# Optimization experiments

Hardware: AMD Instinct MI355X
Metric: run time of the kernel (lower is better)

## Reference

```python
import jax, jax.numpy as jnp
import numpy as np

B, S, D, H = 2, 2048, 2048, 16
HD = D // H


def setup_inputs() -> dict:
    key = jax.random.key(0)
    ks = jax.random.split(key, 9)
    s = 1.0 / np.sqrt(D)
    return {
        "hidden_states": jax.random.normal(ks[0], (B, S, D), dtype=jnp.float32),
        "attention_mask": jnp.ones((B, 1, 1, S), dtype=jnp.int32),
        "Wq": jax.random.normal(ks[1], (D, D), dtype=jnp.float32) * s,
        "bq": jnp.zeros((D,), dtype=jnp.float32),
        "Wk": jax.random.normal(ks[2], (D, D), dtype=jnp.float32) * s,
        "bk": jnp.zeros((D,), dtype=jnp.float32),
        "Wv": jax.random.normal(ks[3], (D, D), dtype=jnp.float32) * s,
        "bv": jnp.zeros((D,), dtype=jnp.float32),
        "Wo": jax.random.normal(ks[4], (D, D), dtype=jnp.float32) * s,
        "bo": jnp.zeros((D,), dtype=jnp.float32),
    }


def reference(hidden_states, attention_mask, Wq, bq, Wk, bk, Wv, bv, Wo, bo):
    scale = 1.0 / np.sqrt(HD)
    # projections: torch Linear is x @ W.T + b
    q = hidden_states @ Wq.T + bq
    k = hidden_states @ Wk.T + bk
    v = hidden_states @ Wv.T + bv
    # [B,S,D] -> [B,H,S,hd]
    q = q.reshape(B, S, H, HD).transpose(0, 2, 1, 3)
    k = k.reshape(B, S, H, HD).transpose(0, 2, 1, 3)
    v = v.reshape(B, S, H, HD).transpose(0, 2, 1, 3)
    scores = jnp.einsum("bhqd,bhkd->bhqk", q, k) * scale
    scores = jnp.where(attention_mask == 0, jnp.float32(-1e9), scores)
    probs = jax.nn.softmax(scores, axis=-1)
    attn = jnp.einsum("bhqk,bhkd->bhqd", probs, v)
    attn = attn.transpose(0, 2, 1, 3).reshape(B, S, D)
    out = attn @ Wo.T + bo
    return out
```

## Files before the change

kernel.cpp:

```cpp
#include <hip/hip_runtime.h>
#include <hip/hip_bf16.h>
#include <stdint.h>

typedef __attribute__((ext_vector_type(8))) short short8;
typedef __attribute__((ext_vector_type(8))) unsigned short ushort8;
typedef __attribute__((ext_vector_type(4))) float f32x4;

#define DEVI __device__ __forceinline__

DEVI unsigned short f2bf(float f) {
    union { float f; unsigned int u; } a;
    a.f = f;
    unsigned int u = a.u;
    u += 0x7fffu + ((u >> 16) & 1u);
    return (unsigned short)(u >> 16);
}

DEVI void stage16(const unsigned short* g, unsigned short* ldsbase) {
    __builtin_amdgcn_global_load_lds(
        (const __attribute__((address_space(1))) void*)(uintptr_t)g,
        (__attribute__((address_space(3))) void*)(uintptr_t)ldsbase,
        16, 0, 0);
}

__global__ void cast_all(const float* __restrict__ hs, const float* __restrict__ wq,
                         const float* __restrict__ wk, const float* __restrict__ wv,
                         const float* __restrict__ wo, unsigned short* __restrict__ dst) {
    int i = blockIdx.x * blockDim.x + threadIdx.x;
    const float* src;
    int local;
    if (i < 1048576) { src = hs; local = i; }
    else {
        int j = i - 1048576;
        int w = j >> 19;
        local = j & 524287;
        src = (w == 0) ? wq : (w == 1) ? wk : (w == 2) ? wv : wo;
    }
    const float4* s = (const float4*)src;
    float4 x = s[2 * local], y = s[2 * local + 1];
    ushort8 o;
    o[0] = f2bf(x.x); o[1] = f2bf(x.y); o[2] = f2bf(x.z); o[3] = f2bf(x.w);
    o[4] = f2bf(y.x); o[5] = f2bf(y.y); o[6] = f2bf(y.z); o[7] = f2bf(y.w);
    *(ushort8*)(dst + 8 * i) = o;
}

#define QSCALE 0.12751879523173862f

__launch_bounds__(256, 3)
__global__ void gemm_qkv(const unsigned short* __restrict__ A, const unsigned short* __restrict__ Bstack,
                         const float* __restrict__ bq, const float* __restrict__ bk,
                         const float* __restrict__ bv, unsigned short* __restrict__ qb,
                         unsigned short* __restrict__ kb, unsigned short* __restrict__ vtb) {
    constexpr int K = 2048;
    __shared__ __align__(16) unsigned short As[2 * 4096];
    __shared__ __align__(16) unsigned short Bs[2 * 4096];
    const int tid = threadIdx.x;
    const int lane = tid & 63, wid = tid >> 6;
    const int quad = lane >> 4, l15 = lane & 15;
    const int m0 = blockIdx.y * 128, n0 = blockIdx.x * 128;
    const int mode = n0 >> 11;
    const int wm = (wid & 1) * 64, wn = (wid >> 1) * 64;

    f32x4 acc[4][4];
#pragma unroll
    for (int i = 0; i < 4; i++)
#pragma unroll
        for (int j = 0; j < 4; j++) acc[i][j] = f32x4{0.f, 0.f, 0.f, 0.f};

    const int s0 = wid * 128 + lane, s1 = s0 + 64;
    const int r0 = s0 >> 2, c0 = (s0 & 3) ^ (r0 & 3);
    const int r1 = s1 >> 2, c1 = (s1 & 3) ^ (r1 & 3);
    const int ldsoffA0 = wid * 1024, ldsoffA1 = wid * 1024 + 512;
    const unsigned short* Ag0 = &A[(m0 + r0) * K + c0 * 8];
    const unsigned short* Ag1 = &A[(m0 + r1) * K + c1 * 8];
    const unsigned short* Bg0 = &Bstack[(n0 + r0) * K + c0 * 8];
    const unsigned short* Bg1 = &Bstack[(n0 + r1) * K + c1 * 8];

    stage16(Ag0, &As[ldsoffA0]);
    stage16(Ag1, &As[ldsoffA1]);
    stage16(Bg0, &Bs[ldsoffA0]);
    stage16(Bg1, &Bs[ldsoffA1]);

    for (int i = 0; i < 64; i++) {
        const int cur = (i & 1) * 4096;
        asm volatile("s_waitcnt vmcnt(0)" ::: "memory");
        __syncthreads();
        if (i < 63) {
            const int nxt = 4096 - cur;
            const int koff = (i + 1) * 32;
            stage16(Ag0 + koff, &As[nxt + ldsoffA0]);
            stage16(Ag1 + koff, &As[nxt + ldsoffA1]);
            stage16(Bg0 + koff, &Bs[nxt + ldsoffA0]);
            stage16(Bg1 + koff, &Bs[nxt + ldsoffA1]);
        }
        short8 af[4], bfr[4];
#pragma unroll
        for (int mi = 0; mi < 4; mi++) {
            int row = wm + mi * 16 + l15;
            int cc = quad ^ (row & 3);
            af[mi] = *(const short8*)&As[cur + row * 32 + cc * 8];
        }
#pragma unroll
        for (int ni = 0; ni < 4; ni++) {
            int row = wn + ni * 16 + l15;
            int cc = quad ^ (row & 3);
            bfr[ni] = *(const short8*)&Bs[cur + row * 32 + cc * 8];
        }
#pragma unroll
        for (int mi = 0; mi < 4; mi++)
#pragma unroll
            for (int ni = 0; ni < 4; ni++)
                acc[mi][ni] = __builtin_amdgcn_mfma_f32_16x16x32_bf16(af[mi], bfr[ni], acc[mi][ni], 0, 0, 0);
    }

    const float* bias = (mode == 0) ? bq : (mode == 1) ? bk : bv;
#pragma unroll
    for (int mi = 0; mi < 4; mi++) {
#pragma unroll
        for (int ni = 0; ni < 4; ni++) {
            int n = n0 + wn + ni * 16 + l15;
            int nl = n & 2047;
            float bb = bias[nl];
            if (mode == 2) {
                int m_base = m0 + wm + mi * 16 + quad * 4;
                int h = nl >> 7, dd = nl & 127, bbb = m_base >> 11, s = m_base & 2047;
                unsigned int v0 = f2bf(acc[mi][ni][0] + bb) | ((unsigned int)f2bf(acc[mi][ni][1] + bb) << 16);
                unsigned int v1 = f2bf(acc[mi][ni][2] + bb) | ((unsigned int)f2bf(acc[mi][ni][3] + bb) << 16);
                uint2 pk; pk.x = v0; pk.y = v1;
                *(uint2*)&vtb[((bbb * 16 + h) * 128 + dd) * 2048 + s] = pk;
            } else {
                unsigned short* dst = (mode == 0) ? qb : kb;
                float sc = (mode == 0) ? QSCALE : 1.0f;
#pragma unroll
                for (int r = 0; r < 4; r++) {
                    int m = m0 + wm + mi * 16 + quad * 4 + r;
                    dst[m * 2048 + nl] = f2bf((acc[mi][ni][r] + bb) * sc);
                }
            }
        }
    }
}

__launch_bounds__(256, 2)
__global__ void gemm_out(const unsigned short* __restrict__ A, const unsigned short* __restrict__ Bw,
                         const float* __restrict__ bias, float* __restrict__ Cout) {
    constexpr int K = 2048;
    __shared__ __align__(16) unsigned short As[2 * 4096];
    __shared__ __align__(16) unsigned short Bs[2 * 4096];
    const int tid = threadIdx.x;
    const int lane = tid & 63, wid = tid >> 6;
    const int quad = lane >> 4, l15 = lane & 15;
    const int m0 = blockIdx.y * 128, n0 = blockIdx.x * 128;
    const int wm = (wid & 1) * 64, wn = (wid >> 1) * 64;

    f32x4 acc[4][4];
#pragma unroll
    for (int i = 0; i < 4; i++)
#pragma unroll
        for (int j = 0; j < 4; j++) acc[i][j] = f32x4{0.f, 0.f, 0.f, 0.f};

    const int s0 = wid * 128 + lane, s1 = s0 + 64;
    const int r0 = s0 >> 2, c0 = (s0 & 3) ^ (r0 & 3);
    const int r1 = s1 >> 2, c1 = (s1 & 3) ^ (r1 & 3);
    const int ldsoffA0 = wid * 1024, ldsoffA1 = wid * 1024 + 512;
    const unsigned short* Ag0 = &A[(m0 + r0) * K + c0 * 8];
    const unsigned short* Ag1 = &A[(m0 + r1) * K + c1 * 8];
    const unsigned short* Bg0 = &Bw[(n0 + r0) * K + c0 * 8];
    const unsigned short* Bg1 = &Bw[(n0 + r1) * K + c1 * 8];

    stage16(Ag0, &As[ldsoffA0]);
    stage16(Ag1, &As[ldsoffA1]);
    stage16(Bg0, &Bs[ldsoffA0]);
    stage16(Bg1, &Bs[ldsoffA1]);

    for (int i = 0; i < 64; i++) {
        const int cur = (i & 1) * 4096;
        asm volatile("s_waitcnt vmcnt(0)" ::: "memory");
        __syncthreads();
        if (i < 63) {
            const int nxt = 4096 - cur;
            const int koff = (i + 1) * 32;
            stage16(Ag0 + koff, &As[nxt + ldsoffA0]);
            stage16(Ag1 + koff, &As[nxt + ldsoffA1]);
            stage16(Bg0 + koff, &Bs[nxt + ldsoffA0]);
            stage16(Bg1 + koff, &Bs[nxt + ldsoffA1]);
        }
        short8 af[4], bfr[4];
#pragma unroll
        for (int mi = 0; mi < 4; mi++) {
            int row = wm + mi * 16 + l15;
            int cc = quad ^ (row & 3);
            af[mi] = *(const short8*)&As[cur + row * 32 + cc * 8];
        }
#pragma unroll
        for (int ni = 0; ni < 4; ni++) {
            int row = wn + ni * 16 + l15;
            int cc = quad ^ (row & 3);
            bfr[ni] = *(const short8*)&Bs[cur + row * 32 + cc * 8];
        }
#pragma unroll
        for (int mi = 0; mi < 4; mi++)
#pragma unroll
            for (int ni = 0; ni < 4; ni++)
                acc[mi][ni] = __builtin_amdgcn_mfma_f32_16x16x32_bf16(af[mi], bfr[ni], acc[mi][ni], 0, 0, 0);
    }

#pragma unroll
    for (int mi = 0; mi < 4; mi++) {
#pragma unroll
        for (int ni = 0; ni < 4; ni++) {
            int n = n0 + wn + ni * 16 + l15;
            float bb = bias[n];
#pragma unroll
            for (int r = 0; r < 4; r++) {
                int m = m0 + wm + mi * 16 + quad * 4 + r;
                Cout[m * 2048 + n] = acc[mi][ni][r] + bb;
            }
        }
    }
}

__launch_bounds__(256, 3)
__global__ void attn_fused(const unsigned short* __restrict__ Q, const unsigned short* __restrict__ Kb,
                           const unsigned short* __restrict__ VT, const int* __restrict__ mask,
                           unsigned short* __restrict__ Ob) {
    __shared__ __align__(16) unsigned short Ks[64 * 128];
    __shared__ __align__(16) unsigned short Vs[128 * 64];
    __shared__ __align__(16) unsigned short Ps[4 * 32 * 72];

    const int tid = threadIdx.x;
    const int lane = tid & 63, wid = tid >> 6;
    const int quad = lane >> 4, l15 = lane & 15;
    const int qt = blockIdx.x, bh = blockIdx.y;
    const int b = bh >> 4, h = bh & 15;
    const int tok0 = b * 2048 + qt * 128 + wid * 32;

    short8 aq[2][4];
#pragma unroll
    for (int mi = 0; mi < 2; mi++)
#pragma unroll
        for (int c = 0; c < 4; c++)
            aq[mi][c] = *(const short8*)&Q[(tok0 + mi * 16 + l15) * 2048 + h * 128 + c * 32 + quad * 8];

    f32x4 oacc[2][8];
#pragma unroll
    for (int mi = 0; mi < 2; mi++)
#pragma unroll
        for (int c = 0; c < 8; c++) oacc[mi][c] = f32x4{0.f, 0.f, 0.f, 0.f};
    float lacc[2][4] = {{0.f, 0.f, 0.f, 0.f}, {0.f, 0.f, 0.f, 0.f}};

    const unsigned short* Kbase = Kb + b * 2048 * 2048 + h * 128;
    const unsigned short* Vbase = VT + (b * 16 + h) * 128 * 2048;

    const unsigned short* KgP[4];
    const unsigned short* VgP[4];
    unsigned short* ldsK[4];
    unsigned short* ldsV[4];
#pragma unroll
    for (int j = 0; j < 4; j++) {
        int s = wid * 256 + j * 64 + lane;
        int kr = s >> 4, kc = (s & 15) ^ (kr & 7);
        int vr = s >> 3, vc = (s & 7) ^ (vr & 7);
        KgP[j] = Kbase + kr * 2048 + kc * 8;
        VgP[j] = Vbase + vr * 2048 + vc * 8;
        ldsK[j] = &Ks[(wid * 256 + j * 64) * 8];
        ldsV[j] = &Vs[(wid * 256 + j * 64) * 8];
    }
    unsigned short* pw = &Ps[wid * 2304];

    for (int kt = 0; kt < 32; kt++) {
        const int key0 = kt * 64;
        __syncthreads();
#pragma unroll
        for (int j = 0; j < 4; j++) {
            stage16(KgP[j] + key0 * 2048, ldsK[j]);
            stage16(VgP[j] + key0, ldsV[j]);
        }
        int mk[4];
#pragma unroll
        for (int t = 0; t < 4; t++) mk[t] = mask[b * 2048 + key0 + t * 16 + l15];
        asm volatile("s_waitcnt vmcnt(0)" ::: "memory");
        __syncthreads();

        f32x4 sc[2][4];
#pragma unroll
        for (int mi = 0; mi < 2; mi++)
#pragma unroll
            for (int t = 0; t < 4; t++) sc[mi][t] = f32x4{0.f, 0.f, 0.f, 0.f};
#pragma unroll
        for (int c = 0; c < 4; c++)
#pragma unroll
            for (int t = 0; t < 4; t++) {
                int row = t * 16 + l15;
                int cc = (4 * c + quad) ^ (row & 7);
                short8 bk = *(const short8*)&Ks[row * 128 + cc * 8];
                sc[0][t] = __builtin_amdgcn_mfma_f32_16x16x32_bf16(aq[0][c], bk, sc[0][t], 0, 0, 0);
                sc[1][t] = __builtin_amdgcn_mfma_f32_16x16x32_bf16(aq[1][c], bk, sc[1][t], 0, 0, 0);
            }

#pragma unroll
        for (int mi = 0; mi < 2; mi++)
#pragma unroll
            for (int t = 0; t < 4; t++)
#pragma unroll
                for (int r = 0; r < 4; r++) {
                    float cs = mk[t] ? sc[mi][t][r] : -1e30f;
                    float p = __builtin_amdgcn_exp2f(cs);
                    lacc[mi][r] += p;
                    pw[(mi * 16 + quad * 4 + r) * 72 + t * 16 + l15] = f2bf(p);
                }
        asm volatile("s_waitcnt lgkmcnt(0)" ::: "memory");
        short8 ap[2][2];
#pragma unroll
        for (int mi = 0; mi < 2; mi++)
#pragma unroll
            for (int kk = 0; kk < 2; kk++)
                ap[mi][kk] = *(const short8*)&pw[(mi * 16 + l15) * 72 + kk * 32 + quad * 8];

#pragma unroll
        for (int kk = 0; kk < 2; kk++)
#pragma unroll
            for (int dt = 0; dt < 8; dt++) {
                int row = dt * 16 + l15;
                int cc = (kk * 4 + quad) ^ (row & 7);
                short8 bv = *(const short8*)&Vs[row * 64 + cc * 8];
                oacc[0][dt] = __builtin_amdgcn_mfma_f32_16x16x32_bf16(ap[0][kk], bv, oacc[0][dt], 0, 0, 0);
                oacc[1][dt] = __builtin_amdgcn_mfma_f32_16x16x32_bf16(ap[1][kk], bv, oacc[1][dt], 0, 0, 0);
            }
    }

    float inv[2][4];
#pragma unroll
    for (int mi = 0; mi < 2; mi++)
#pragma unroll
        for (int r = 0; r < 4; r++) {
            float l = lacc[mi][r];
#pragma unroll
            for (int off = 1; off < 16; off <<= 1) l += __shfl_xor(l, off, 64);
            inv[mi][r] = 1.0f / l;
        }
#pragma unroll
    for (int mi = 0; mi < 2; mi++)
#pragma unroll
        for (int dt = 0; dt < 8; dt++)
#pragma unroll
            for (int r = 0; r < 4; r++) {
                float val = oacc[mi][dt][r] * inv[mi][r];
                Ob[(tok0 + mi * 16 + quad * 4 + r) * 2048 + h * 128 + dt * 16 + l15] = f2bf(val);
            }
}

extern "C" void kernel_launch(void* const* d_in, const int* in_sizes, int n_in,
                              void* d_out, int out_size, void* d_ws, size_t ws_size,
                              hipStream_t stream) {
    const float* hs = (const float*)d_in[0];
    const int* mask = (const int*)d_in[1];
    const float* Wq = (const float*)d_in[2];
    const float* bq = (const float*)d_in[3];
    const float* Wk = (const float*)d_in[4];
    const float* bk = (const float*)d_in[5];
    const float* Wv = (const float*)d_in[6];
    const float* bv = (const float*)d_in[7];
    const float* Wo = (const float*)d_in[8];
    const float* bo = (const float*)d_in[9];

    unsigned short* hsb = (unsigned short*)d_ws;
    unsigned short* wqb = hsb + 8388608;
    unsigned short* wob = wqb + 3 * 4194304;
    unsigned short* qb  = wob + 4194304;
    unsigned short* kb  = qb  + 8388608;
    unsigned short* vtb = kb  + 8388608;
    unsigned short* ab  = vtb + 8388608;

    unsigned short* wkb = wqb + 4194304;
    unsigned short* wvb = wkb + 4194304;
    (void)wkb; (void)wvb;

    cast_all<<<12288, 256, 0, stream>>>(hs, Wq, Wk, Wv, Wo, hsb);

    gemm_qkv<<<dim3(48, 32), 256, 0, stream>>>(hsb, wqb, bq, bk, bv, qb, kb, vtb);
    attn_fused<<<dim3(16, 32), 256, 0, stream>>>(qb, kb, vtb, mask, ab);
    gemm_out<<<dim3(16, 32), 256, 0, stream>>>(ab, wob, bo, (float*)d_out);
}
```

Baseline: 466.7 us.

## Double-buffer K/V tiles in attention with 512-thread blocks and LDS-cached mask

```diff
diff --git a/kernel.cpp b/kernel.cpp
--- a/kernel.cpp
+++ b/kernel.cpp
@@ -220,20 +220,23 @@
     }
 }
 
-__launch_bounds__(256, 3)
+__launch_bounds__(512, 1)
 __global__ void attn_fused(const unsigned short* __restrict__ Q, const unsigned short* __restrict__ Kb,
                            const unsigned short* __restrict__ VT, const int* __restrict__ mask,
                            unsigned short* __restrict__ Ob) {
-    __shared__ __align__(16) unsigned short Ks[64 * 128];
-    __shared__ __align__(16) unsigned short Vs[128 * 64];
-    __shared__ __align__(16) unsigned short Ps[4 * 32 * 72];
+    __shared__ __align__(16) unsigned short Ks[2][64 * 128];
+    __shared__ __align__(16) unsigned short Vs[2][128 * 64];
+    __shared__ __align__(16) unsigned short Ps[8][32 * 72];
+    __shared__ int Ms[2048];
 
     const int tid = threadIdx.x;
     const int lane = tid & 63, wid = tid >> 6;
     const int quad = lane >> 4, l15 = lane & 15;
     const int qt = blockIdx.x, bh = blockIdx.y;
     const int b = bh >> 4, h = bh & 15;
-    const int tok0 = b * 2048 + qt * 128 + wid * 32;
+    const int tok0 = b * 2048 + qt * 256 + wid * 32;
+
+    for (int i = tid; i < 2048; i += 512) Ms[i] = mask[b * 2048 + i];
 
     short8 aq[2][4];
 #pragma unroll
@@ -252,35 +255,44 @@
     const unsigned short* Kbase = Kb + b * 2048 * 2048 + h * 128;
     const unsigned short* Vbase = VT + (b * 16 + h) * 128 * 2048;
 
-    const unsigned short* KgP[4];
-    const unsigned short* VgP[4];
-    unsigned short* ldsK[4];
-    unsigned short* ldsV[4];
-#pragma unroll
-    for (int j = 0; j < 4; j++) {
-        int s = wid * 256 + j * 64 + lane;
+    const unsigned short* KgP[2];
+    const unsigned short* VgP[2];
+    int ldsKoff[2], ldsVoff[2];
+#pragma unroll
+    for (int j = 0; j < 2; j++) {
+        int s = wid * 128 + j * 64 + lane;
         int kr = s >> 4, kc = (s & 15) ^ (kr & 7);
         int vr = s >> 3, vc = (s & 7) ^ (vr & 7);
         KgP[j] = Kbase + kr * 2048 + kc * 8;
         VgP[j] = Vbase + vr * 2048 + vc * 8;
-        ldsK[j] = &Ks[(wid * 256 + j * 64) * 8];
-        ldsV[j] = &Vs[(wid * 256 + j * 64) * 8];
-    }
-    unsigned short* pw = &Ps[wid * 2304];
+        ldsKoff[j] = (wid * 128 + j * 64) * 8;
+        ldsVoff[j] = (wid * 128 + j * 64) * 8;
+    }
+    unsigned short* pw = &Ps[wid][0];
+
+#pragma unroll
+    for (int j = 0; j < 2; j++) {
+        stage16(KgP[j], &Ks[0][ldsKoff[j]]);
+        stage16(VgP[j], &Vs[0][ldsVoff[j]]);
+    }
 
     for (int kt = 0; kt < 32; kt++) {
+        const int cur = kt & 1;
         const int key0 = kt * 64;
-        __syncthreads();
-#pragma unroll
-        for (int j = 0; j < 4; j++) {
-            stage16(KgP[j] + key0 * 2048, ldsK[j]);
-            stage16(VgP[j] + key0, ldsV[j]);
-        }
-        int mk[4];
-#pragma unroll
-        for (int t = 0; t < 4; t++) mk[t] = mask[b * 2048 + key0 + t * 16 + l15];
         asm volatile("s_waitcnt vmcnt(0)" ::: "memory");
         __syncthreads();
+        if (kt < 31) {
+            const int nb = cur ^ 1;
+            const int key0n = key0 + 64;
+#pragma unroll
+            for (int j = 0; j < 2; j++) {
+                stage16(KgP[j] + key0n * 2048, &Ks[nb][ldsKoff[j]]);
+                stage16(VgP[j] + key0n, &Vs[nb][ldsVoff[j]]);
+            }
+        }
+        int mk[4];
+#pragma unroll
+        for (int t = 0; t < 4; t++) mk[t] = Ms[key0 + t * 16 + l15];
 
         f32x4 sc[2][4];
 #pragma unroll
@@ -293,7 +305,7 @@
             for (int t = 0; t < 4; t++) {
                 int row = t * 16 + l15;
                 int cc = (4 * c + quad) ^ (row & 7);
-                short8 bk = *(const short8*)&Ks[row * 128 + cc * 8];
+                short8 bk = *(const short8*)&Ks[cur][row * 128 + cc * 8];
                 sc[0][t] = __builtin_amdgcn_mfma_f32_16x16x32_bf16(aq[0][c], bk, sc[0][t], 0, 0, 0);
                 sc[1][t] = __builtin_amdgcn_mfma_f32_16x16x32_bf16(aq[1][c], bk, sc[1][t], 0, 0, 0);
             }
@@ -323,7 +335,7 @@
             for (int dt = 0; dt < 8; dt++) {
                 int row = dt * 16 + l15;
                 int cc = (kk * 4 + quad) ^ (row & 7);
-                short8 bv = *(const short8*)&Vs[row * 64 + cc * 8];
+                short8 bv = *(const short8*)&Vs[cur][row * 64 + cc * 8];
                 oacc[0][dt] = __builtin_amdgcn_mfma_f32_16x16x32_bf16(ap[0][kk], bv, oacc[0][dt], 0, 0, 0);
                 oacc[1][dt] = __builtin_amdgcn_mfma_f32_16x16x32_bf16(ap[1][kk], bv, oacc[1][dt], 0, 0, 0);
             }
@@ -372,13 +384,9 @@
     unsigned short* vtb = kb  + 8388608;
     unsigned short* ab  = vtb + 8388608;
 
-    unsigned short* wkb = wqb + 4194304;
-    unsigned short* wvb = wkb + 4194304;
-    (void)wkb; (void)wvb;
-
     cast_all<<<12288, 256, 0, stream>>>(hs, Wq, Wk, Wv, Wo, hsb);
 
     gemm_qkv<<<dim3(48, 32), 256, 0, stream>>>(hsb, wqb, bq, bk, bv, qb, kb, vtb);
-    attn_fused<<<dim3(16, 32), 256, 0, stream>>>(qb, kb, vtb, mask, ab);
+    attn_fused<<<dim3(8, 32), 512, 0, stream>>>(qb, kb, vtb, mask, ab);
     gemm_out<<<dim3(16, 32), 256, 0, stream>>>(ab, wob, bo, (float*)d_out);
 }
```

New measurement: 400.5 us. 14.2% less time.
